# Performance work log

Measured on AMD Instinct MI355X. Metric: run time of the kernel, lower is better.

Reference implementation:

```python
import jax, jax.numpy as jnp
import numpy as np

B, S, D = 32768, 16, 64


def setup_inputs() -> dict:
    key = jax.random.key(0)
    k1, k2, k3, k4 = jax.random.split(key, 4)
    z1 = jax.random.normal(k1, (B, S, D), dtype=jnp.float32)
    z2 = jax.random.normal(k2, (B, S, D), dtype=jnp.float32)
    a = jax.random.uniform(k3, (), dtype=jnp.float32)          # constrained to [0,1]
    b = jax.random.normal(k4, (), dtype=jnp.float32)
    return {"z1": z1, "z2": z2, "a": a, "b": b}


def reference(z1, z2, a, b):
    # Pairwise Euclidean distances between the S MC samples of z1 and z2
    # per batch element: dist[b, i, j] = ||z1[b,i] - z2[b,j]||_2.
    sq1 = jnp.sum(z1 * z1, axis=-1)                    # [B, S]
    sq2 = jnp.sum(z2 * z2, axis=-1)                    # [B, S]
    dots = jnp.einsum('bid,bjd->bij', z1, z2)          # [B, S, S]
    d2 = sq1[:, :, None] + sq2[:, None, :] - 2.0 * dots
    dist = jnp.sqrt(jnp.maximum(d2, 0.0))              # [B, S, S]
    # Original concatenates over samples -> [B, S*S] (then squeeze).
    dist = dist.reshape(dist.shape[0], -1)             # [B, S*S]
    logit = jax.nn.sigmoid(dist * a + b)
    return jnp.clip(logit, 1e-08, 1.0)
```

## Files before the change

### kernel.cpp

```cpp
#include <hip/hip_runtime.h>
#include <math.h>

#define Bn 32768
#define Sn 16
#define Dn 64
#define NB 2
#define STRIDE 68
#define THREADS 128

__global__ __launch_bounds__(THREADS, 4)
void get_logit_mc_kernel(const float* __restrict__ z1,
                         const float* __restrict__ z2,
                         const float* __restrict__ pa,
                         const float* __restrict__ pb,
                         float* __restrict__ out) {
    __shared__ float zs[2][NB][Sn][STRIDE];

    const int t  = threadIdx.x;
    const int bb = blockIdx.x * NB;

    #pragma unroll
    for (int k = 0; k < 8; ++k) {
        int Q     = t + k * THREADS;
        int batch = Q >> 9;
        int rem   = Q & 511;
        int arr   = rem >> 8;
        int e     = rem & 255;
        int row   = e >> 4;
        int q     = e & 15;
        const float* src = (arr ? z2 : z1) +
                           (((size_t)(bb + batch) * Sn + row) * Dn + q * 4);
        float4 v = *reinterpret_cast<const float4*>(src);
        *reinterpret_cast<float4*>(&zs[arr][batch][row][q * 4]) = v;
    }

    const float av = pa[0];
    const float bv = pb[0];

    __syncthreads();

    const int bl = t >> 6;
    const int r  = (t >> 3) & 7;
    const int c  = t & 7;

    float acc[2][2] = {{0.f,0.f},{0.f,0.f}};

    #pragma unroll
    for (int q = 0; q < 16; ++q) {
        float4 x0 = *reinterpret_cast<const float4*>(&zs[0][bl][2*r    ][q*4]);
        float4 x1 = *reinterpret_cast<const float4*>(&zs[0][bl][2*r + 1][q*4]);
        #pragma unroll
        for (int jj = 0; jj < 2; ++jj) {
            float4 y = *reinterpret_cast<const float4*>(&zs[1][bl][2*c + jj][q*4]);
            float d;
            d = x0.x - y.x; acc[0][jj] = fmaf(d, d, acc[0][jj]);
            d = x0.y - y.y; acc[0][jj] = fmaf(d, d, acc[0][jj]);
            d = x0.z - y.z; acc[0][jj] = fmaf(d, d, acc[0][jj]);
            d = x0.w - y.w; acc[0][jj] = fmaf(d, d, acc[0][jj]);
            d = x1.x - y.x; acc[1][jj] = fmaf(d, d, acc[1][jj]);
            d = x1.y - y.y; acc[1][jj] = fmaf(d, d, acc[1][jj]);
            d = x1.z - y.z; acc[1][jj] = fmaf(d, d, acc[1][jj]);
            d = x1.w - y.w; acc[1][jj] = fmaf(d, d, acc[1][jj]);
        }
    }

    #pragma unroll
    for (int ii = 0; ii < 2; ++ii) {
        float2 o;
        #pragma unroll
        for (int jj = 0; jj < 2; ++jj) {
            float dist = sqrtf(acc[ii][jj]);
            float x    = fmaf(dist, av, bv);
            float e    = __expf(-x);
            float sg   = 1.0f / (1.0f + e);
            sg = fminf(sg, 1.0f);
            sg = fmaxf(sg, 1e-8f);
            (&o.x)[jj] = sg;
        }
        int i = 2*r + ii;
        float* dst = out + ((size_t)(bb + bl) * (Sn * Sn) + i * Sn + c * 2);
        *reinterpret_cast<float2*>(dst) = o;
    }
}

extern "C" void kernel_launch(void* const* d_in, const int* in_sizes, int n_in,
                              void* d_out, int out_size, void* d_ws, size_t ws_size,
                              hipStream_t stream) {
    const float* z1 = (const float*)d_in[0];
    const float* z2 = (const float*)d_in[1];
    const float* pa = (const float*)d_in[2];
    const float* pb = (const float*)d_in[3];
    float* out      = (float*)d_out;

    dim3 grid(Bn / NB);
    dim3 block(THREADS);
    hipLaunchKernelGGL(get_logit_mc_kernel, grid, block, 0, stream,
                       z1, z2, pa, pb, out);
}
```

Before: 52.61 us.

## Make blocks persistent over four batch tiles with register-prefetched next tile

Each block now processes four consecutive pairs of batch elements instead of one. While the current tile is being computed from shared memory, the global loads for the next tile are issued into registers, so memory latency overlaps with compute. The grid shrinks by four, and each tile adds an extra barrier. Fewer blocks and the added register pressure could reduce occupancy and the latency hiding that came from running many blocks at once.

```diff
diff --git a/kernel.cpp b/kernel.cpp
--- a/kernel.cpp
+++ b/kernel.cpp
@@ -7,6 +7,7 @@
 #define NB 2
 #define STRIDE 68
 #define THREADS 128
+#define TPB 4
 
 __global__ __launch_bounds__(THREADS, 4)
 void get_logit_mc_kernel(const float* __restrict__ z1,
@@ -16,70 +17,97 @@
                          float* __restrict__ out) {
     __shared__ float zs[2][NB][Sn][STRIDE];
 
-    const int t  = threadIdx.x;
-    const int bb = blockIdx.x * NB;
+    const int t   = threadIdx.x;
+    const int bb0 = blockIdx.x * (NB * TPB);
+
+    const float av = pa[0];
+    const float bv = pb[0];
+
+    const int bl = t >> 6;
+    const int r  = (t >> 3) & 7;
+    const int c  = t & 7;
+
+    float4 regs[8];
 
     #pragma unroll
     for (int k = 0; k < 8; ++k) {
         int Q     = t + k * THREADS;
         int batch = Q >> 9;
-        int rem   = Q & 511;
-        int arr   = rem >> 8;
-        int e     = rem & 255;
-        int row   = e >> 4;
-        int q     = e & 15;
+        int arr   = (Q >> 8) & 1;
+        int row   = (Q >> 4) & 15;
+        int q     = Q & 15;
         const float* src = (arr ? z2 : z1) +
-                           (((size_t)(bb + batch) * Sn + row) * Dn + q * 4);
-        float4 v = *reinterpret_cast<const float4*>(src);
-        *reinterpret_cast<float4*>(&zs[arr][batch][row][q * 4]) = v;
+            (((size_t)(bb0 + batch) * Sn + row) * Dn + q * 4);
+        regs[k] = *reinterpret_cast<const float4*>(src);
     }
 
-    const float av = pa[0];
-    const float bv = pb[0];
+    for (int tt = 0; tt < TPB; ++tt) {
+        #pragma unroll
+        for (int k = 0; k < 8; ++k) {
+            int Q     = t + k * THREADS;
+            int batch = Q >> 9;
+            int arr   = (Q >> 8) & 1;
+            int row   = (Q >> 4) & 15;
+            int q     = Q & 15;
+            *reinterpret_cast<float4*>(&zs[arr][batch][row][q * 4]) = regs[k];
+        }
+        __syncthreads();
 
-    __syncthreads();
+        if (tt + 1 < TPB) {
+            const int bbn = bb0 + (tt + 1) * NB;
+            #pragma unroll
+            for (int k = 0; k < 8; ++k) {
+                int Q     = t + k * THREADS;
+                int batch = Q >> 9;
+                int arr   = (Q >> 8) & 1;
+                int row   = (Q >> 4) & 15;
+                int q     = Q & 15;
+                const float* src = (arr ? z2 : z1) +
+                    (((size_t)(bbn + batch) * Sn + row) * Dn + q * 4);
+                regs[k] = *reinterpret_cast<const float4*>(src);
+            }
+        }
 
-    const int bl = t >> 6;
-    const int r  = (t >> 3) & 7;
-    const int c  = t & 7;
+        float acc[2][2] = {{0.f,0.f},{0.f,0.f}};
+        #pragma unroll
+        for (int q = 0; q < 16; ++q) {
+            float4 x0 = *reinterpret_cast<const float4*>(&zs[0][bl][2*r    ][q*4]);
+            float4 x1 = *reinterpret_cast<const float4*>(&zs[0][bl][2*r + 1][q*4]);
+            #pragma unroll
+            for (int jj = 0; jj < 2; ++jj) {
+                float4 y = *reinterpret_cast<const float4*>(&zs[1][bl][2*c + jj][q*4]);
+                float d;
+                d = x0.x - y.x; acc[0][jj] = fmaf(d, d, acc[0][jj]);
+                d = x0.y - y.y; acc[0][jj] = fmaf(d, d, acc[0][jj]);
+                d = x0.z - y.z; acc[0][jj] = fmaf(d, d, acc[0][jj]);
+                d = x0.w - y.w; acc[0][jj] = fmaf(d, d, acc[0][jj]);
+                d = x1.x - y.x; acc[1][jj] = fmaf(d, d, acc[1][jj]);
+                d = x1.y - y.y; acc[1][jj] = fmaf(d, d, acc[1][jj]);
+                d = x1.z - y.z; acc[1][jj] = fmaf(d, d, acc[1][jj]);
+                d = x1.w - y.w; acc[1][jj] = fmaf(d, d, acc[1][jj]);
+            }
+        }
 
-    float acc[2][2] = {{0.f,0.f},{0.f,0.f}};
+        const int gb = bb0 + tt * NB + bl;
+        #pragma unroll
+        for (int ii = 0; ii < 2; ++ii) {
+            float2 o;
+            #pragma unroll
+            for (int jj = 0; jj < 2; ++jj) {
+                float dist = sqrtf(acc[ii][jj]);
+                float x    = fmaf(dist, av, bv);
+                float e    = __expf(-x);
+                float sg   = 1.0f / (1.0f + e);
+                sg = fminf(sg, 1.0f);
+                sg = fmaxf(sg, 1e-8f);
+                (&o.x)[jj] = sg;
+            }
+            int i = 2*r + ii;
+            float* dst = out + ((size_t)gb * (Sn * Sn) + i * Sn + c * 2);
+            *reinterpret_cast<float2*>(dst) = o;
+        }
 
-    #pragma unroll
-    for (int q = 0; q < 16; ++q) {
-        float4 x0 = *reinterpret_cast<const float4*>(&zs[0][bl][2*r    ][q*4]);
-        float4 x1 = *reinterpret_cast<const float4*>(&zs[0][bl][2*r + 1][q*4]);
-        #pragma unroll
-        for (int jj = 0; jj < 2; ++jj) {
-            float4 y = *reinterpret_cast<const float4*>(&zs[1][bl][2*c + jj][q*4]);
-            float d;
-            d = x0.x - y.x; acc[0][jj] = fmaf(d, d, acc[0][jj]);
-            d = x0.y - y.y; acc[0][jj] = fmaf(d, d, acc[0][jj]);
-            d = x0.z - y.z; acc[0][jj] = fmaf(d, d, acc[0][jj]);
-            d = x0.w - y.w; acc[0][jj] = fmaf(d, d, acc[0][jj]);
-            d = x1.x - y.x; acc[1][jj] = fmaf(d, d, acc[1][jj]);
-            d = x1.y - y.y; acc[1][jj] = fmaf(d, d, acc[1][jj]);
-            d = x1.z - y.z; acc[1][jj] = fmaf(d, d, acc[1][jj]);
-            d = x1.w - y.w; acc[1][jj] = fmaf(d, d, acc[1][jj]);
-        }
-    }
-
-    #pragma unroll
-    for (int ii = 0; ii < 2; ++ii) {
-        float2 o;
-        #pragma unroll
-        for (int jj = 0; jj < 2; ++jj) {
-            float dist = sqrtf(acc[ii][jj]);
-            float x    = fmaf(dist, av, bv);
-            float e    = __expf(-x);
-            float sg   = 1.0f / (1.0f + e);
-            sg = fminf(sg, 1.0f);
-            sg = fmaxf(sg, 1e-8f);
-            (&o.x)[jj] = sg;
-        }
-        int i = 2*r + ii;
-        float* dst = out + ((size_t)(bb + bl) * (Sn * Sn) + i * Sn + c * 2);
-        *reinterpret_cast<float2*>(dst) = o;
+        __syncthreads();
     }
 }
 
@@ -92,7 +120,7 @@
     const float* pb = (const float*)d_in[3];
     float* out      = (float*)d_out;
 
-    dim3 grid(Bn / NB);
+    dim3 grid(Bn / (NB * TPB));
     dim3 block(THREADS);
     hipLaunchKernelGGL(get_logit_mc_kernel, grid, block, 0, stream,
                        z1, z2, pa, pb, out);
```

After: 148.5 us. +182.2%, slower.
